# Performance work log

Measured on AMD Instinct MI355X. Metric: run time of the kernel, lower is better.

## Reference

```python
import jax, jax.numpy as jnp
import numpy as np

B, H, S, D = 2, 8, 2048, 64
WINDOW = 3            # local_attention_window (default in torch forward)
FRAC = 0.3            # percentage_frac hardcoded in create_window_tensor call
MASK_FILL = -1.0e9


def window_kernel(window, frac):
    # create_window_tensor: [ (1-f)^n ... (1-f)^1, 1, (1-f)^1 ... (1-f)^n ]
    n = (window - 1) // 2
    side = np.array([(1.0 - frac) ** i for i in range(n, 0, -1)], dtype=np.float32)
    vals = np.concatenate([side, np.array([1.0], np.float32), side[::-1]])
    return jnp.asarray(vals)


def setup_inputs() -> dict:
    key = jax.random.key(0)
    kq, kk, kv = jax.random.split(key, 3)
    queries = jax.random.normal(kq, (B, H, S, D), jnp.float32)
    keys = jax.random.normal(kk, (B, H, S, D), jnp.float32)
    values = jax.random.normal(kv, (B, H, S, D), jnp.float32)
    # causal mask: True positions are filled with -1e9 (masked_fill semantics)
    mask = jnp.triu(jnp.ones((S, S), dtype=bool), 1)[None, None]  # [1,1,S,S]
    # linear_bias: nn.Parameter(torch.zeros(Sk)) created inside forward
    beta = jnp.zeros((S,), jnp.float32)
    return {"queries": queries, "keys": keys, "values": values,
            "beta": beta, "mask": mask}


def reference(queries, keys, values, beta, mask):
    d = keys.shape[-1]
    # scores = Q K^T / sqrt(d)
    scores = jnp.einsum("bhqd,bhkd->bhqk", queries, keys) / jnp.sqrt(
        jnp.asarray(d, queries.dtype))
    scores = jnp.where(mask, jnp.asarray(MASK_FILL, scores.dtype), scores)
    # include_local_attention=True, local_attention_dim_vertical=False:
    # the torch code transposes, conv2d with a [1,W] kernel along the last
    # axis, transposes back -> 1D cross-correlation along the QUERY axis.
    # Kernel is symmetric so correlation == convolution. Zero padding.
    kern = window_kernel(WINDOW, FRAC)
    p = (WINDOW - 1) // 2
    xp = jnp.pad(scores, ((0, 0), (0, 0), (p, p), (0, 0)))
    Sq = scores.shape[2]
    scores = sum(kern[i] * jax.lax.dynamic_slice_in_dim(xp, i, Sq, axis=2)
                 for i in range(WINDOW))
    # linear_bias=True: add zero-initialized per-key-position bias
    scores = scores + beta  # broadcasts over last dim [Sk]
    weights = jax.nn.softmax(scores, axis=-1)
    return jnp.einsum("bhqk,bhkd->bhqd", weights, values)
```

## Files before the change

kernel.cpp:

```cpp
#include <hip/hip_runtime.h>


typedef short bf16x8 __attribute__((ext_vector_type(8)));
typedef float f32x4  __attribute__((ext_vector_type(4)));

constexpr int S_ = 2048;
constexpr int D_ = 64;
constexpr float LOG2E = 1.44269504088896341f;
constexpr float KSC = 0.125f * LOG2E;

__device__ __forceinline__ unsigned pk2(float lo, float hi) {
    union { float f; unsigned u; } a, b;
    a.f = lo; b.f = hi;
    return __builtin_amdgcn_perm(b.u + 0x8000u, a.u + 0x8000u, 0x07060302u);
}

__global__ __launch_bounds__(256)
void cvt8(const float* __restrict__ K, const float* __restrict__ V,
          unsigned short* __restrict__ F)
{
    __shared__ float T[64][68];

    const int bid = blockIdx.x;
    const int hd = bid & 15, tt = bid >> 4;
    const float* Kt = K + ((size_t)hd * S_ + tt * 64) * D_;
    const float* Vt = V + ((size_t)hd * S_ + tt * 64) * D_;
    unsigned short* Ft = F + (size_t)(hd * 32 + tt) * 8192;

    const int t = threadIdx.x;
    const int key = t >> 2, d0 = (t & 3) << 4;

    {
        const float* vp = Vt + key * D_ + d0;
        #pragma unroll
        for (int i = 0; i < 4; ++i) {
            float4 v4 = *(const float4*)(vp + 4 * i);
            T[d0 + 4 * i + 0][key] = v4.x;
            T[d0 + 4 * i + 1][key] = v4.y;
            T[d0 + 4 * i + 2][key] = v4.z;
            T[d0 + 4 * i + 3][key] = v4.w;
        }
    }

    {
        const float* kp = Kt + key * D_ + d0;
        float4 a = *(const float4*)(kp);
        float4 b = *(const float4*)(kp + 4);
        float4 c = *(const float4*)(kp + 8);
        float4 d = *(const float4*)(kp + 12);
        uint4 w0 = make_uint4(pk2(a.x, a.y), pk2(a.z, a.w), pk2(b.x, b.y), pk2(b.z, b.w));
        uint4 w1 = make_uint4(pk2(c.x, c.y), pk2(c.z, c.w), pk2(d.x, d.y), pk2(d.z, d.w));
        const int r5 = key & 31;
        const int kh = key >> 5, mb = (r5 >> 2) & 1;
        const int n = ((r5 >> 3) << 2) | (r5 & 3);
        const int hh = d0 >> 5, qd0 = (d0 >> 3) & 3;
        const int f0 = (kh << 2) | (mb << 1) | hh;
        *(uint4*)(Ft + f0 * 512 + ((qd0 << 4) | n) * 8)       = w0;
        *(uint4*)(Ft + f0 * 512 + (((qd0 + 1) << 4) | n) * 8) = w1;
    }
    __syncthreads();

    #pragma unroll
    for (int s = 0; s < 2; ++s) {
        const int slot = t + s * 256;
        const int fr = slot >> 6, lane = slot & 63;
        const int kh = fr >> 2, mb = fr & 3, n = lane & 15, qd = lane >> 4;
        const float* row = &T[mb * 16 + n][kh * 32 + qd * 8];
        uint4 w = make_uint4(pk2(row[0], row[1]), pk2(row[2], row[3]),
                             pk2(row[4], row[5]), pk2(row[6], row[7]));
        *(uint4*)(Ft + (8 + fr) * 512 + lane * 8) = w;
    }
}

__global__ __launch_bounds__(512, 2)
void attn8(const float* __restrict__ Q, const float* __restrict__ beta,
           const unsigned short* __restrict__ F, float* __restrict__ out)
{
    __shared__ float opub[4][16][68];
    __shared__ float lred[4][16];

    const int bid = blockIdx.x;
    const int hd = bid & 15;
    const int pr = bid >> 4;

    const float* Qh = Q + (size_t)hd * S_ * D_;
    const unsigned short* Fh = F + (size_t)hd * 32 * 8192;

    const int t = threadIdx.x, lane = t & 63;
    const int wv = t >> 6, kh = wv & 1, sg = wv >> 1;
    const int n_l = lane & 15, qd = lane >> 4;

    const int lo = lane * 8;
    int kfo[2][2], vfo[4];
    #pragma unroll
    for (int mb = 0; mb < 2; ++mb)
        #pragma unroll
        for (int hh = 0; hh < 2; ++hh)
            kfo[mb][hh] = ((kh << 2) | (mb << 1) | hh) * 512 + lo;
    #pragma unroll
    for (int mb = 0; mb < 4; ++mb)
        vfo[mb] = (8 + (kh << 2) + mb) * 512 + lo;

    const int kvo = (kh << 5) + (qd << 3);
    const float* bp = beta + kvo;

    for (int p = 0; p < 2; ++p) {
        const int j = p ? (31 - pr) : pr;
        const int q0 = j << 6;
        const int nt = j + 1;
        const int qbase = q0 + (sg << 4);
        const int qr = qbase + n_l;

        auto ld = [&](int tile, bf16x8 (&ka)[2][2], bf16x8 (&vb)[4], float (&bt)[8]) {
            const unsigned short* fp = Fh + (size_t)tile * 8192;
            ka[0][0] = *(const bf16x8*)(fp + kfo[0][0]);
            ka[0][1] = *(const bf16x8*)(fp + kfo[0][1]);
            ka[1][0] = *(const bf16x8*)(fp + kfo[1][0]);
            ka[1][1] = *(const bf16x8*)(fp + kfo[1][1]);
            #pragma unroll
            for (int mb = 0; mb < 4; ++mb)
                vb[mb] = *(const bf16x8*)(fp + vfo[mb]);
            const float* bq = bp + (tile << 6);
            float4 b0 = *(const float4*)(bq);
            float4 b1 = *(const float4*)(bq + 4);
            bt[0] = b0.x * LOG2E; bt[1] = b0.y * LOG2E;
            bt[2] = b0.z * LOG2E; bt[3] = b0.w * LOG2E;
            bt[4] = b1.x * LOG2E; bt[5] = b1.y * LOG2E;
            bt[6] = b1.z * LOG2E; bt[7] = b1.w * LOG2E;
        };

        bf16x8 kaA[2][2], vbA[4]; float btA[8];
        bf16x8 kaB[2][2], vbB[4]; float btB[8];
        bf16x8 kaC[2][2], vbC[4]; float btC[8];
        ld(0, kaA, vbA, btA);
        if (nt > 1) ld(1, kaB, vbB, btB);

        bf16x8 qb[2];
        {
            const float wp = (qr > 0) ? 0.7f : 0.0f;
            const float wn = (qr + 1 < S_) ? 0.7f : 0.0f;
            const float* qc = Qh + (size_t)qr * D_;
            const float* qpp = qc - ((qr > 0) ? D_ : 0);
            const float* qnn = qc + ((qr + 1 < S_) ? D_ : 0);
            #pragma unroll
            for (int hh = 0; hh < 2; ++hh) {
                const int d0 = (hh << 5) + (qd << 3);
                float4 c0 = *(const float4*)(qc + d0),  c1 = *(const float4*)(qc + d0 + 4);
                float4 p0 = *(const float4*)(qpp + d0), p1 = *(const float4*)(qpp + d0 + 4);
                float4 n0 = *(const float4*)(qnn + d0), n1 = *(const float4*)(qnn + d0 + 4);
                float e0 = fmaf(wn, n0.x, fmaf(wp, p0.x, c0.x));
                float e1 = fmaf(wn, n0.y, fmaf(wp, p0.y, c0.y));
                float e2 = fmaf(wn, n0.z, fmaf(wp, p0.z, c0.z));
                float e3 = fmaf(wn, n0.w, fmaf(wp, p0.w, c0.w));
                float e4 = fmaf(wn, n1.x, fmaf(wp, p1.x, c1.x));
                float e5 = fmaf(wn, n1.y, fmaf(wp, p1.y, c1.y));
                float e6 = fmaf(wn, n1.z, fmaf(wp, p1.z, c1.z));
                float e7 = fmaf(wn, n1.w, fmaf(wp, p1.w, c1.w));
                union { unsigned u[4]; bf16x8 v; } qu;
                qu.u[0] = pk2(e0, e1); qu.u[1] = pk2(e2, e3);
                qu.u[2] = pk2(e4, e5); qu.u[3] = pk2(e6, e7);
                qb[hh] = qu.v;
            }
        }

        f32x4 o[4];
        float l = 0.0f;
        #pragma unroll
        for (int mb = 0; mb < 4; ++mb) o[mb] = (f32x4){0, 0, 0, 0};

        auto comp = [&](int tile, bf16x8 (&ka)[2][2], bf16x8 (&vb)[4], float (&bt)[8]) {
            const f32x4 zz = {0, 0, 0, 0};
            f32x4 acc[2];
            #pragma unroll
            for (int mb = 0; mb < 2; ++mb) {
                f32x4 a = __builtin_amdgcn_mfma_f32_16x16x32_bf16(ka[mb][0], qb[0], zz, 0, 0, 0);
                acc[mb] = __builtin_amdgcn_mfma_f32_16x16x32_bf16(ka[mb][1], qb[1], a, 0, 0, 0);
            }
            const bool dm = (tile == nt - 1);
            const int kk = (tile << 6) + kvo;
            float pv[8];
            float la = 0.0f;
            #pragma unroll
            for (int jj = 0; jj < 8; ++jj) {
                const int mb = jj >> 2, r = jj & 3;
                float sv = fmaf(acc[mb][r], KSC, bt[jj]);
                if (dm) {
                    const int key = kk + jj;
                    if (!((key < qr) || (qr == 0 && key == 0))) sv = -1.0e30f;
                }
                pv[jj] = __builtin_amdgcn_exp2f(sv);
                la += pv[jj];
            }
            l += la;
            union { unsigned u[4]; bf16x8 v; } pf;
            pf.u[0] = pk2(pv[0], pv[1]);
            pf.u[1] = pk2(pv[2], pv[3]);
            pf.u[2] = pk2(pv[4], pv[5]);
            pf.u[3] = pk2(pv[6], pv[7]);
            #pragma unroll
            for (int mb = 0; mb < 4; ++mb)
                o[mb] = __builtin_amdgcn_mfma_f32_16x16x32_bf16(vb[mb], pf.v, o[mb], 0, 0, 0);
        };

        int it = 0;
        for (; it + 3 <= nt; it += 3) {
            ld(it + 2, kaC, vbC, btC);
            comp(it, kaA, vbA, btA);
            if (it + 3 < nt) ld(it + 3, kaA, vbA, btA);
            comp(it + 1, kaB, vbB, btB);
            if (it + 4 < nt) ld(it + 4, kaB, vbB, btB);
            comp(it + 2, kaC, vbC, btC);
        }
        if (it < nt)     comp(it, kaA, vbA, btA);
        if (it + 1 < nt) comp(it + 1, kaB, vbB, btB);

        l += __shfl_xor(l, 16);
        l += __shfl_xor(l, 32);
        __syncthreads();
        if (kh == 0) {
            #pragma unroll
            for (int mb = 0; mb < 4; ++mb)
                *(float4*)&opub[sg][n_l][(mb << 4) + (qd << 2)] =
                    make_float4(o[mb][0], o[mb][1], o[mb][2], o[mb][3]);
            if (qd == 0) lred[sg][n_l] = l;
        }
        __syncthreads();
        if (kh == 1) {
            const float inv = 1.0f / (l + lred[sg][n_l]);
            float* op = out + ((size_t)hd * S_ + qr) * D_ + (qd << 2);
            #pragma unroll
            for (int mb = 0; mb < 4; ++mb) {
                float4 pv = *(float4*)&opub[sg][n_l][(mb << 4) + (qd << 2)];
                *(float4*)(op + (mb << 4)) =
                    make_float4((o[mb][0] + pv.x) * inv, (o[mb][1] + pv.y) * inv,
                                (o[mb][2] + pv.z) * inv, (o[mb][3] + pv.w) * inv);
            }
        }
    }
}

extern "C" void kernel_launch(void* const* d_in, const int* in_sizes, int n_in,
                              void* d_out, int out_size, void* d_ws, size_t ws_size,
                              hipStream_t stream) {
    const float* Q    = (const float*)d_in[0];
    const float* K    = (const float*)d_in[1];
    const float* V    = (const float*)d_in[2];
    const float* beta = (const float*)d_in[3];
    float* out = (float*)d_out;

    unsigned short* F = (unsigned short*)d_ws;

    cvt8<<<dim3(512), 256, 0, stream>>>(K, V, F);
    attn8<<<dim3(256), 512, 0, stream>>>(Q, beta, F, out);
}
```

Measured before the change: 118.2 us.

## Give each wave two query groups and split key tiles by parity

Waves now each handle 32 query rows (two 16-row groups) and one key half, and the key tiles are split between wave pairs by parity. Each loaded K/V fragment is reused across two MFMA query groups, so per-wave global loads per unit of work are halved. Partial outputs from the four wave combinations are combined through a larger shared slab in two reduction stages. The cost is more accumulator registers, an extra barrier, and a shallower double buffer in place of the old triple buffer.

```diff
diff --git a/kernel.cpp b/kernel.cpp
--- a/kernel.cpp
+++ b/kernel.cpp
@@ -73,11 +73,10 @@
 }
 
 __global__ __launch_bounds__(512, 2)
-void attn8(const float* __restrict__ Q, const float* __restrict__ beta,
+void attn9(const float* __restrict__ Q, const float* __restrict__ beta,
            const unsigned short* __restrict__ F, float* __restrict__ out)
 {
-    __shared__ float opub[4][16][68];
-    __shared__ float lred[4][16];
+    __shared__ float slab[2][64][72];
 
     const int bid = blockIdx.x;
     const int hd = bid & 15;
@@ -87,7 +86,8 @@
     const unsigned short* Fh = F + (size_t)hd * 32 * 8192;
 
     const int t = threadIdx.x, lane = t & 63;
-    const int wv = t >> 6, kh = wv & 1, sg = wv >> 1;
+    const int wv = t >> 6;
+    const int kh = wv & 1, par = (wv >> 1) & 1, qh = wv >> 2;
     const int n_l = lane & 15, qd = lane >> 4;
 
     const int lo = lane * 8;
@@ -108,8 +108,7 @@
         const int j = p ? (31 - pr) : pr;
         const int q0 = j << 6;
         const int nt = j + 1;
-        const int qbase = q0 + (sg << 4);
-        const int qr = qbase + n_l;
+        const int qbase = q0 + (qh << 5);
 
         auto ld = [&](int tile, bf16x8 (&ka)[2][2], bf16x8 (&vb)[4], float (&bt)[8]) {
             const unsigned short* fp = Fh + (size_t)tile * 8192;
@@ -129,19 +128,15 @@
             bt[6] = b1.z * LOG2E; bt[7] = b1.w * LOG2E;
         };
 
-        bf16x8 kaA[2][2], vbA[4]; float btA[8];
-        bf16x8 kaB[2][2], vbB[4]; float btB[8];
-        bf16x8 kaC[2][2], vbC[4]; float btC[8];
-        ld(0, kaA, vbA, btA);
-        if (nt > 1) ld(1, kaB, vbB, btB);
-
-        bf16x8 qb[2];
-        {
-            const float wp = (qr > 0) ? 0.7f : 0.0f;
-            const float wn = (qr + 1 < S_) ? 0.7f : 0.0f;
-            const float* qc = Qh + (size_t)qr * D_;
-            const float* qpp = qc - ((qr > 0) ? D_ : 0);
-            const float* qnn = qc + ((qr + 1 < S_) ? D_ : 0);
+        bf16x8 qb[2][2];
+        #pragma unroll
+        for (int ng = 0; ng < 2; ++ng) {
+            const int q = qbase + (ng << 4) + n_l;
+            const float wp = (q > 0) ? 0.7f : 0.0f;
+            const float wn = (q + 1 < S_) ? 0.7f : 0.0f;
+            const float* qc = Qh + (size_t)q * D_;
+            const float* qpp = qc - ((q > 0) ? D_ : 0);
+            const float* qnn = qc + ((q + 1 < S_) ? D_ : 0);
             #pragma unroll
             for (int hh = 0; hh < 2; ++hh) {
                 const int d0 = (hh << 5) + (qd << 3);
@@ -159,81 +154,128 @@
                 union { unsigned u[4]; bf16x8 v; } qu;
                 qu.u[0] = pk2(e0, e1); qu.u[1] = pk2(e2, e3);
                 qu.u[2] = pk2(e4, e5); qu.u[3] = pk2(e6, e7);
-                qb[hh] = qu.v;
-            }
-        }
-
-        f32x4 o[4];
-        float l = 0.0f;
-        #pragma unroll
-        for (int mb = 0; mb < 4; ++mb) o[mb] = (f32x4){0, 0, 0, 0};
+                qb[ng][hh] = qu.v;
+            }
+        }
+
+        f32x4 o[4][2];
+        float l[2] = {0.0f, 0.0f};
+        #pragma unroll
+        for (int mb = 0; mb < 4; ++mb)
+            #pragma unroll
+            for (int ng = 0; ng < 2; ++ng) o[mb][ng] = (f32x4){0, 0, 0, 0};
 
         auto comp = [&](int tile, bf16x8 (&ka)[2][2], bf16x8 (&vb)[4], float (&bt)[8]) {
             const f32x4 zz = {0, 0, 0, 0};
-            f32x4 acc[2];
-            #pragma unroll
-            for (int mb = 0; mb < 2; ++mb) {
-                f32x4 a = __builtin_amdgcn_mfma_f32_16x16x32_bf16(ka[mb][0], qb[0], zz, 0, 0, 0);
-                acc[mb] = __builtin_amdgcn_mfma_f32_16x16x32_bf16(ka[mb][1], qb[1], a, 0, 0, 0);
-            }
+            f32x4 acc[2][2];
+            #pragma unroll
+            for (int mb = 0; mb < 2; ++mb)
+                #pragma unroll
+                for (int ng = 0; ng < 2; ++ng) {
+                    f32x4 a = __builtin_amdgcn_mfma_f32_16x16x32_bf16(ka[mb][0], qb[ng][0], zz, 0, 0, 0);
+                    acc[mb][ng] = __builtin_amdgcn_mfma_f32_16x16x32_bf16(ka[mb][1], qb[ng][1], a, 0, 0, 0);
+                }
             const bool dm = (tile == nt - 1);
             const int kk = (tile << 6) + kvo;
-            float pv[8];
-            float la = 0.0f;
-            #pragma unroll
-            for (int jj = 0; jj < 8; ++jj) {
-                const int mb = jj >> 2, r = jj & 3;
-                float sv = fmaf(acc[mb][r], KSC, bt[jj]);
-                if (dm) {
-                    const int key = kk + jj;
-                    if (!((key < qr) || (qr == 0 && key == 0))) sv = -1.0e30f;
-                }
-                pv[jj] = __builtin_amdgcn_exp2f(sv);
-                la += pv[jj];
-            }
-            l += la;
-            union { unsigned u[4]; bf16x8 v; } pf;
-            pf.u[0] = pk2(pv[0], pv[1]);
-            pf.u[1] = pk2(pv[2], pv[3]);
-            pf.u[2] = pk2(pv[4], pv[5]);
-            pf.u[3] = pk2(pv[6], pv[7]);
+            union { unsigned u[4]; bf16x8 v; } pf[2];
+            #pragma unroll
+            for (int ng = 0; ng < 2; ++ng) {
+                const int qr = qbase + (ng << 4) + n_l;
+                float pv[8];
+                float la = 0.0f;
+                #pragma unroll
+                for (int jj = 0; jj < 8; ++jj) {
+                    const int mb = jj >> 2, r = jj & 3;
+                    float sv = fmaf(acc[mb][ng][r], KSC, bt[jj]);
+                    if (dm) {
+                        const int key = kk + jj;
+                        if (!((key < qr) || (qr == 0 && key == 0))) sv = -1.0e30f;
+                    }
+                    pv[jj] = __builtin_amdgcn_exp2f(sv);
+                    la += pv[jj];
+                }
+                l[ng] += la;
+                pf[ng].u[0] = pk2(pv[0], pv[1]);
+                pf[ng].u[1] = pk2(pv[2], pv[3]);
+                pf[ng].u[2] = pk2(pv[4], pv[5]);
+                pf[ng].u[3] = pk2(pv[6], pv[7]);
+            }
             #pragma unroll
             for (int mb = 0; mb < 4; ++mb)
-                o[mb] = __builtin_amdgcn_mfma_f32_16x16x32_bf16(vb[mb], pf.v, o[mb], 0, 0, 0);
+                #pragma unroll
+                for (int ng = 0; ng < 2; ++ng)
+                    o[mb][ng] = __builtin_amdgcn_mfma_f32_16x16x32_bf16(vb[mb], pf[ng].v, o[mb][ng], 0, 0, 0);
         };
 
-        int it = 0;
-        for (; it + 3 <= nt; it += 3) {
-            ld(it + 2, kaC, vbC, btC);
+        bf16x8 kaA[2][2], vbA[4]; float btA[8];
+        bf16x8 kaB[2][2], vbB[4]; float btB[8];
+        int it = par;
+        if (it < nt) {
+            ld(it, kaA, vbA, btA);
+            if (it + 2 < nt) ld(it + 2, kaB, vbB, btB);
+            while (it + 4 < nt) {
+                comp(it, kaA, vbA, btA);
+                ld(it + 4, kaA, vbA, btA);
+                comp(it + 2, kaB, vbB, btB);
+                if (it + 6 < nt) ld(it + 6, kaB, vbB, btB);
+                it += 4;
+            }
             comp(it, kaA, vbA, btA);
-            if (it + 3 < nt) ld(it + 3, kaA, vbA, btA);
-            comp(it + 1, kaB, vbB, btB);
-            if (it + 4 < nt) ld(it + 4, kaB, vbB, btB);
-            comp(it + 2, kaC, vbC, btC);
-        }
-        if (it < nt)     comp(it, kaA, vbA, btA);
-        if (it + 1 < nt) comp(it + 1, kaB, vbB, btB);
-
-        l += __shfl_xor(l, 16);
-        l += __shfl_xor(l, 32);
+            if (it + 2 < nt) comp(it + 2, kaB, vbB, btB);
+        }
+
+        #pragma unroll
+        for (int ng = 0; ng < 2; ++ng) {
+            l[ng] += __shfl_xor(l[ng], 16);
+            l[ng] += __shfl_xor(l[ng], 32);
+        }
         __syncthreads();
-        if (kh == 0) {
-            #pragma unroll
-            for (int mb = 0; mb < 4; ++mb)
-                *(float4*)&opub[sg][n_l][(mb << 4) + (qd << 2)] =
-                    make_float4(o[mb][0], o[mb][1], o[mb][2], o[mb][3]);
-            if (qd == 0) lred[sg][n_l] = l;
+        if (par == 1) {
+            #pragma unroll
+            for (int ng = 0; ng < 2; ++ng) {
+                const int row = (qh << 5) + (ng << 4) + n_l;
+                #pragma unroll
+                for (int mb = 0; mb < 4; ++mb)
+                    *(float4*)&slab[kh][row][(mb << 4) + (qd << 2)] =
+                        make_float4(o[mb][ng][0], o[mb][ng][1], o[mb][ng][2], o[mb][ng][3]);
+                if (qd == 0) slab[kh][row][64] = l[ng];
+            }
         }
         __syncthreads();
-        if (kh == 1) {
-            const float inv = 1.0f / (l + lred[sg][n_l]);
-            float* op = out + ((size_t)hd * S_ + qr) * D_ + (qd << 2);
-            #pragma unroll
-            for (int mb = 0; mb < 4; ++mb) {
-                float4 pv = *(float4*)&opub[sg][n_l][(mb << 4) + (qd << 2)];
-                *(float4*)(op + (mb << 4)) =
-                    make_float4((o[mb][0] + pv.x) * inv, (o[mb][1] + pv.y) * inv,
-                                (o[mb][2] + pv.z) * inv, (o[mb][3] + pv.w) * inv);
+        if (par == 0) {
+            #pragma unroll
+            for (int ng = 0; ng < 2; ++ng) {
+                const int row = (qh << 5) + (ng << 4) + n_l;
+                #pragma unroll
+                for (int mb = 0; mb < 4; ++mb) {
+                    float4 pv4 = *(float4*)&slab[kh][row][(mb << 4) + (qd << 2)];
+                    o[mb][ng][0] += pv4.x; o[mb][ng][1] += pv4.y;
+                    o[mb][ng][2] += pv4.z; o[mb][ng][3] += pv4.w;
+                }
+                l[ng] += slab[kh][row][64];
+                if (kh == 0) {
+                    #pragma unroll
+                    for (int mb = 0; mb < 4; ++mb)
+                        *(float4*)&slab[0][row][(mb << 4) + (qd << 2)] =
+                            make_float4(o[mb][ng][0], o[mb][ng][1], o[mb][ng][2], o[mb][ng][3]);
+                    if (qd == 0) slab[0][row][64] = l[ng];
+                }
+            }
+        }
+        __syncthreads();
+        if (par == 0 && kh == 1) {
+            #pragma unroll
+            for (int ng = 0; ng < 2; ++ng) {
+                const int row = (qh << 5) + (ng << 4) + n_l;
+                const float inv = 1.0f / (l[ng] + slab[0][row][64]);
+                float* op = out + ((size_t)hd * S_ + q0 + row) * D_ + (qd << 2);
+                #pragma unroll
+                for (int mb = 0; mb < 4; ++mb) {
+                    float4 pv4 = *(float4*)&slab[0][row][(mb << 4) + (qd << 2)];
+                    *(float4*)(op + (mb << 4)) =
+                        make_float4((o[mb][ng][0] + pv4.x) * inv, (o[mb][ng][1] + pv4.y) * inv,
+                                    (o[mb][ng][2] + pv4.z) * inv, (o[mb][ng][3] + pv4.w) * inv);
+                }
             }
         }
     }
@@ -251,5 +293,5 @@
     unsigned short* F = (unsigned short*)d_ws;
 
     cvt8<<<dim3(512), 256, 0, stream>>>(K, V, F);
-    attn8<<<dim3(256), 512, 0, stream>>>(Q, beta, F, out);
-}
+    attn9<<<dim3(256), 512, 0, stream>>>(Q, beta, F, out);
+}
```

Result: no change. 117.5 us (-0.6%).

## Split query tiles across more blocks and interleave key tiles between wave pairs

Applied to the files above, without the earlier changes.

Doubles the grid so each block handles 32 query rows of a 64-row tile. Within a block, waves split the key tiles by parity as well as by key half. Partial outputs and row sums are combined through a shared slab in a two-stage reduction. The K prefetch is narrowed to a two-deep ring, with V and bias loaded inside the compute step. P is packed to bf16 by truncation instead of rounding, and the occupancy hint is raised to 4 blocks per SM. This trades more parallelism and lower register pressure for extra synchronisation, an extra reduction stage, less prefetch depth for V, and slightly less accurate P.

```diff
diff --git a/kernel.cpp b/kernel.cpp
--- a/kernel.cpp
+++ b/kernel.cpp
@@ -13,6 +13,11 @@
     union { float f; unsigned u; } a, b;
     a.f = lo; b.f = hi;
     return __builtin_amdgcn_perm(b.u + 0x8000u, a.u + 0x8000u, 0x07060302u);
+}
+__device__ __forceinline__ unsigned pk2t(float lo, float hi) {
+    union { float f; unsigned u; } a, b;
+    a.f = lo; b.f = hi;
+    return __builtin_amdgcn_perm(b.u, a.u, 0x07060302u);
 }
 
 __global__ __launch_bounds__(256)
@@ -72,22 +77,24 @@
     }
 }
 
-__global__ __launch_bounds__(512, 2)
-void attn8(const float* __restrict__ Q, const float* __restrict__ beta,
-           const unsigned short* __restrict__ F, float* __restrict__ out)
+__global__ __launch_bounds__(512, 4)
+void attn10(const float* __restrict__ Q, const float* __restrict__ beta,
+            const unsigned short* __restrict__ F, float* __restrict__ out)
 {
-    __shared__ float opub[4][16][68];
-    __shared__ float lred[4][16];
+    __shared__ float slab[2][32][72];
 
     const int bid = blockIdx.x;
     const int hd = bid & 15;
-    const int pr = bid >> 4;
+    const int sb = bid >> 4;
+    const int pr = sb >> 1;
+    const int hf = sb & 1;
 
     const float* Qh = Q + (size_t)hd * S_ * D_;
     const unsigned short* Fh = F + (size_t)hd * 32 * 8192;
 
     const int t = threadIdx.x, lane = t & 63;
-    const int wv = t >> 6, kh = wv & 1, sg = wv >> 1;
+    const int wv = t >> 6;
+    const int kh = wv & 1, par = (wv >> 1) & 1, qh = wv >> 2;
     const int n_l = lane & 15, qd = lane >> 4;
 
     const int lo = lane * 8;
@@ -106,34 +113,9 @@
 
     for (int p = 0; p < 2; ++p) {
         const int j = p ? (31 - pr) : pr;
-        const int q0 = j << 6;
         const int nt = j + 1;
-        const int qbase = q0 + (sg << 4);
-        const int qr = qbase + n_l;
-
-        auto ld = [&](int tile, bf16x8 (&ka)[2][2], bf16x8 (&vb)[4], float (&bt)[8]) {
-            const unsigned short* fp = Fh + (size_t)tile * 8192;
-            ka[0][0] = *(const bf16x8*)(fp + kfo[0][0]);
-            ka[0][1] = *(const bf16x8*)(fp + kfo[0][1]);
-            ka[1][0] = *(const bf16x8*)(fp + kfo[1][0]);
-            ka[1][1] = *(const bf16x8*)(fp + kfo[1][1]);
-            #pragma unroll
-            for (int mb = 0; mb < 4; ++mb)
-                vb[mb] = *(const bf16x8*)(fp + vfo[mb]);
-            const float* bq = bp + (tile << 6);
-            float4 b0 = *(const float4*)(bq);
-            float4 b1 = *(const float4*)(bq + 4);
-            bt[0] = b0.x * LOG2E; bt[1] = b0.y * LOG2E;
-            bt[2] = b0.z * LOG2E; bt[3] = b0.w * LOG2E;
-            bt[4] = b1.x * LOG2E; bt[5] = b1.y * LOG2E;
-            bt[6] = b1.z * LOG2E; bt[7] = b1.w * LOG2E;
-        };
-
-        bf16x8 kaA[2][2], vbA[4]; float btA[8];
-        bf16x8 kaB[2][2], vbB[4]; float btB[8];
-        bf16x8 kaC[2][2], vbC[4]; float btC[8];
-        ld(0, kaA, vbA, btA);
-        if (nt > 1) ld(1, kaB, vbB, btB);
+        const int q0 = (j << 6) + (hf << 5);
+        const int qr = q0 + (qh << 4) + n_l;
 
         bf16x8 qb[2];
         {
@@ -168,22 +150,41 @@
         #pragma unroll
         for (int mb = 0; mb < 4; ++mb) o[mb] = (f32x4){0, 0, 0, 0};
 
-        auto comp = [&](int tile, bf16x8 (&ka)[2][2], bf16x8 (&vb)[4], float (&bt)[8]) {
+        auto ldk = [&](int tile, bf16x8 (&ka)[2][2]) {
+            const unsigned short* fp = Fh + (size_t)tile * 8192;
+            ka[0][0] = *(const bf16x8*)(fp + kfo[0][0]);
+            ka[0][1] = *(const bf16x8*)(fp + kfo[0][1]);
+            ka[1][0] = *(const bf16x8*)(fp + kfo[1][0]);
+            ka[1][1] = *(const bf16x8*)(fp + kfo[1][1]);
+        };
+
+        auto comp = [&](int tile, bf16x8 (&ka)[2][2]) {
+            const unsigned short* fp = Fh + (size_t)tile * 8192;
+            bf16x8 vb0 = *(const bf16x8*)(fp + vfo[0]);
+            bf16x8 vb1 = *(const bf16x8*)(fp + vfo[1]);
+            bf16x8 vb2 = *(const bf16x8*)(fp + vfo[2]);
+            bf16x8 vb3 = *(const bf16x8*)(fp + vfo[3]);
+            const float* bq = bp + (tile << 6);
+            const float4 b0 = *(const float4*)(bq);
+            const float4 b1 = *(const float4*)(bq + 4);
+
             const f32x4 zz = {0, 0, 0, 0};
-            f32x4 acc[2];
-            #pragma unroll
-            for (int mb = 0; mb < 2; ++mb) {
-                f32x4 a = __builtin_amdgcn_mfma_f32_16x16x32_bf16(ka[mb][0], qb[0], zz, 0, 0, 0);
-                acc[mb] = __builtin_amdgcn_mfma_f32_16x16x32_bf16(ka[mb][1], qb[1], a, 0, 0, 0);
-            }
+            f32x4 a0 = __builtin_amdgcn_mfma_f32_16x16x32_bf16(ka[0][0], qb[0], zz, 0, 0, 0);
+            a0 = __builtin_amdgcn_mfma_f32_16x16x32_bf16(ka[0][1], qb[1], a0, 0, 0, 0);
+            f32x4 a1 = __builtin_amdgcn_mfma_f32_16x16x32_bf16(ka[1][0], qb[0], zz, 0, 0, 0);
+            a1 = __builtin_amdgcn_mfma_f32_16x16x32_bf16(ka[1][1], qb[1], a1, 0, 0, 0);
+
+            const float bt[8] = {b0.x * LOG2E, b0.y * LOG2E, b0.z * LOG2E, b0.w * LOG2E,
+                                 b1.x * LOG2E, b1.y * LOG2E, b1.z * LOG2E, b1.w * LOG2E};
             const bool dm = (tile == nt - 1);
             const int kk = (tile << 6) + kvo;
+
             float pv[8];
             float la = 0.0f;
             #pragma unroll
             for (int jj = 0; jj < 8; ++jj) {
                 const int mb = jj >> 2, r = jj & 3;
-                float sv = fmaf(acc[mb][r], KSC, bt[jj]);
+                float sv = fmaf((mb ? a1[r] : a0[r]), KSC, bt[jj]);
                 if (dm) {
                     const int key = kk + jj;
                     if (!((key < qr) || (qr == 0 && key == 0))) sv = -1.0e30f;
@@ -192,48 +193,73 @@
                 la += pv[jj];
             }
             l += la;
+
             union { unsigned u[4]; bf16x8 v; } pf;
-            pf.u[0] = pk2(pv[0], pv[1]);
-            pf.u[1] = pk2(pv[2], pv[3]);
-            pf.u[2] = pk2(pv[4], pv[5]);
-            pf.u[3] = pk2(pv[6], pv[7]);
-            #pragma unroll
-            for (int mb = 0; mb < 4; ++mb)
-                o[mb] = __builtin_amdgcn_mfma_f32_16x16x32_bf16(vb[mb], pf.v, o[mb], 0, 0, 0);
+            pf.u[0] = pk2t(pv[0], pv[1]);
+            pf.u[1] = pk2t(pv[2], pv[3]);
+            pf.u[2] = pk2t(pv[4], pv[5]);
+            pf.u[3] = pk2t(pv[6], pv[7]);
+
+            o[0] = __builtin_amdgcn_mfma_f32_16x16x32_bf16(vb0, pf.v, o[0], 0, 0, 0);
+            o[1] = __builtin_amdgcn_mfma_f32_16x16x32_bf16(vb1, pf.v, o[1], 0, 0, 0);
+            o[2] = __builtin_amdgcn_mfma_f32_16x16x32_bf16(vb2, pf.v, o[2], 0, 0, 0);
+            o[3] = __builtin_amdgcn_mfma_f32_16x16x32_bf16(vb3, pf.v, o[3], 0, 0, 0);
         };
 
-        int it = 0;
-        for (; it + 3 <= nt; it += 3) {
-            ld(it + 2, kaC, vbC, btC);
-            comp(it, kaA, vbA, btA);
-            if (it + 3 < nt) ld(it + 3, kaA, vbA, btA);
-            comp(it + 1, kaB, vbB, btB);
-            if (it + 4 < nt) ld(it + 4, kaB, vbB, btB);
-            comp(it + 2, kaC, vbC, btC);
-        }
-        if (it < nt)     comp(it, kaA, vbA, btA);
-        if (it + 1 < nt) comp(it + 1, kaB, vbB, btB);
+        bf16x8 kaA[2][2], kaB[2][2];
+        int it = par;
+        if (it < nt) {
+            ldk(it, kaA);
+            if (it + 2 < nt) ldk(it + 2, kaB);
+            while (it + 4 < nt) {
+                comp(it, kaA);
+                ldk(it + 4, kaA);
+                comp(it + 2, kaB);
+                if (it + 6 < nt) ldk(it + 6, kaB);
+                it += 4;
+            }
+            comp(it, kaA);
+            if (it + 2 < nt) comp(it + 2, kaB);
+        }
 
         l += __shfl_xor(l, 16);
         l += __shfl_xor(l, 32);
         __syncthreads();
-        if (kh == 0) {
+        const int row = (qh << 4) + n_l;
+        if (par == 1) {
             #pragma unroll
             for (int mb = 0; mb < 4; ++mb)
-                *(float4*)&opub[sg][n_l][(mb << 4) + (qd << 2)] =
+                *(float4*)&slab[kh][row][(mb << 4) + (qd << 2)] =
                     make_float4(o[mb][0], o[mb][1], o[mb][2], o[mb][3]);
-            if (qd == 0) lred[sg][n_l] = l;
+            if (qd == 0) slab[kh][row][64] = l;
         }
         __syncthreads();
-        if (kh == 1) {
-            const float inv = 1.0f / (l + lred[sg][n_l]);
-            float* op = out + ((size_t)hd * S_ + qr) * D_ + (qd << 2);
+        if (par == 0) {
             #pragma unroll
             for (int mb = 0; mb < 4; ++mb) {
-                float4 pv = *(float4*)&opub[sg][n_l][(mb << 4) + (qd << 2)];
+                float4 pv4 = *(float4*)&slab[kh][row][(mb << 4) + (qd << 2)];
+                o[mb][0] += pv4.x; o[mb][1] += pv4.y;
+                o[mb][2] += pv4.z; o[mb][3] += pv4.w;
+            }
+            l += slab[kh][row][64];
+            if (kh == 1) {
+                #pragma unroll
+                for (int mb = 0; mb < 4; ++mb)
+                    *(float4*)&slab[1][row][(mb << 4) + (qd << 2)] =
+                        make_float4(o[mb][0], o[mb][1], o[mb][2], o[mb][3]);
+                if (qd == 0) slab[1][row][64] = l;
+            }
+        }
+        __syncthreads();
+        if (par == 0 && kh == 0) {
+            const float inv = 1.0f / (l + slab[1][row][64]);
+            float* op = out + ((size_t)hd * S_ + q0 + row) * D_ + (qd << 2);
+            #pragma unroll
+            for (int mb = 0; mb < 4; ++mb) {
+                float4 pv4 = *(float4*)&slab[1][row][(mb << 4) + (qd << 2)];
                 *(float4*)(op + (mb << 4)) =
-                    make_float4((o[mb][0] + pv.x) * inv, (o[mb][1] + pv.y) * inv,
-                                (o[mb][2] + pv.z) * inv, (o[mb][3] + pv.w) * inv);
+                    make_float4((o[mb][0] + pv4.x) * inv, (o[mb][1] + pv4.y) * inv,
+                                (o[mb][2] + pv4.z) * inv, (o[mb][3] + pv4.w) * inv);
             }
         }
     }
@@ -251,5 +277,5 @@
     unsigned short* F = (unsigned short*)d_ws;
 
     cvt8<<<dim3(512), 256, 0, stream>>>(K, V, F);
-    attn8<<<dim3(256), 512, 0, stream>>>(Q, beta, F, out);
-}
+    attn10<<<dim3(512), 512, 0, stream>>>(Q, beta, F, out);
+}
```

New measurement: 133.5 us. 12.9% more time.
